# Optimization experiments

Hardware: AMD Instinct MI355X
Metric: run time of the kernel (lower is better)

The kernel has to match this reference:

```python
import jax, jax.numpy as jnp
import numpy as np
from jax import lax

BN_EPS = 1e-3  # Keras BatchNormalization default


def ste_sign(x):
    # larq ste_sign forward: +1 for x >= 0, -1 otherwise
    return jnp.where(x >= 0, 1.0, -1.0).astype(x.dtype)


def conv2d_valid(x, w):
    # x: NHWC, w: HWIO, stride 1, VALID padding
    return lax.conv_general_dilated(
        x, w, window_strides=(1, 1), padding='VALID',
        dimension_numbers=('NHWC', 'HWIO', 'NHWC'))


def maxpool2(x):
    return lax.reduce_window(x, -jnp.inf, lax.max,
                             (1, 2, 2, 1), (1, 2, 2, 1), 'VALID')


def bn_infer(x, mean, var, beta):
    # BatchNormalization(scale=False): center only
    return (x - mean) * lax.rsqrt(var + BN_EPS) + beta


def setup_inputs() -> dict:
    key = jax.random.key(0)
    ks = jax.random.split(key, 16)
    B, H, W, C = 256, 64, 64, 3
    inp = {
        'inputs': jax.random.normal(ks[0], (B, H, W, C), jnp.float32),
        'w1': jax.random.normal(ks[1], (3, 3, 3, 32), jnp.float32) * 0.1,
        'w2': jax.random.normal(ks[2], (3, 3, 32, 64), jnp.float32) * 0.1,
        'w3': jax.random.normal(ks[3], (3, 3, 64, 64), jnp.float32) * 0.1,
        'd1w': jax.random.normal(ks[4], (12 * 12 * 64, 64), jnp.float32) * 0.05,
        'd2w': jax.random.normal(ks[5], (64, 10), jnp.float32) * 0.1,
    }
    for i, (name, c) in enumerate([('bn1', 32), ('bn2', 64), ('bn3', 64), ('bn4', 64), ('bn5', 10)]):
        kk = jax.random.split(ks[6 + i], 3)
        inp[name + '_mean'] = jax.random.normal(kk[0], (c,), jnp.float32) * 0.1
        inp[name + '_var'] = jax.random.uniform(kk[1], (c,), jnp.float32, 0.5, 1.5)
        inp[name + '_beta'] = jax.random.normal(kk[2], (c,), jnp.float32) * 0.1
    return inp


def reference(inputs, w1, w2, w3, d1w, d2w,
              bn1_mean, bn1_var, bn1_beta,
              bn2_mean, bn2_var, bn2_beta,
              bn3_mean, bn3_var, bn3_beta,
              bn4_mean, bn4_var, bn4_beta,
              bn5_mean, bn5_var, bn5_beta):
    # conv1: kernel quantized only (no input quantizer)
    x = conv2d_valid(inputs, ste_sign(w1))           # [B,62,62,32]
    x = maxpool2(x)                                   # [B,31,31,32]
    x = bn_infer(x, bn1_mean, bn1_var, bn1_beta)
    # conv2: input + kernel quantized
    x = conv2d_valid(ste_sign(x), ste_sign(w2))       # [B,29,29,64]
    x = maxpool2(x)                                   # [B,14,14,64]
    x = bn_infer(x, bn2_mean, bn2_var, bn2_beta)
    x = conv2d_valid(ste_sign(x), ste_sign(w3))       # [B,12,12,64]
    x = bn_infer(x, bn3_mean, bn3_var, bn3_beta)
    x = x.reshape(x.shape[0], -1)                     # [B,9216]
    x = ste_sign(x) @ ste_sign(d1w)                   # [B,64]
    x = bn_infer(x, bn4_mean, bn4_var, bn4_beta)
    x = ste_sign(x) @ ste_sign(d2w)                   # [B,10]
    x = bn_infer(x, bn5_mean, bn5_var, bn5_beta)
    return jax.nn.softmax(x, axis=-1)
```

## Files before the change

kernel.cpp:

```cpp
#include <hip/hip_runtime.h>

typedef unsigned int u32;
typedef unsigned long long u64;

#define BN_EPS 1e-3f

static const size_t OFF_BITS1 = 0;
static const size_t OFF_BITS2 = 984064;
static const size_t OFF_W2B   = 1682432;
static const size_t OFF_W3B   = 1684736;
static const size_t OFF_D1WB  = 1689344;
static const size_t OFF_D2WB  = 1763072;
static const size_t OFF_T2    = 1763328;
static const size_t OFF_T3    = 1763584;
static const size_t OFF_T4    = 1763840;

__global__ __launch_bounds__(256) void k_head(
    const float* __restrict__ inp, const float* __restrict__ w1,
    const float* __restrict__ m1, const float* __restrict__ v1, const float* __restrict__ be1,
    const float* __restrict__ w2, const float* __restrict__ w3,
    const float* __restrict__ d1w, const float* __restrict__ d2w,
    const float* __restrict__ m2, const float* __restrict__ v2, const float* __restrict__ be2,
    const float* __restrict__ m3, const float* __restrict__ v3, const float* __restrict__ be3,
    const float* __restrict__ m4, const float* __restrict__ v4, const float* __restrict__ be4,
    u32* __restrict__ bits1,
    u32* __restrict__ w2b, u64* __restrict__ w3b, u64* __restrict__ d1wb,
    u64* __restrict__ d2wb, float* __restrict__ t2, float* __restrict__ t3,
    float* __restrict__ t4)
{
    int tid = threadIdx.x;

    if (blockIdx.x >= 961) {
        int pb = blockIdx.x - 961;
        if (pb < 36) {
            int idx = pb * 256 + tid;
            int wi = idx >> 6, oc = idx & 63;
            u64 bits = 0;
            for (int j = 0; j < 64; ++j)
                bits |= (u64)(d1w[(wi * 64 + j) * 64 + oc] >= 0.f) << j;
            d1wb[idx] = bits;
        } else if (pb < 39) {
            int idx = (pb - 36) * 256 + tid;
            if (idx < 576) {
                int tap = idx >> 6, oc = idx & 63;
                u32 bits = 0;
                for (int ic = 0; ic < 32; ++ic)
                    bits |= (u32)(w2[(tap * 32 + ic) * 64 + oc] >= 0.f) << ic;
                w2b[idx] = bits;
            }
        } else if (pb < 42) {
            int idx = (pb - 39) * 256 + tid;
            if (idx < 576) {
                int tap = idx >> 6, oc = idx & 63;
                u64 bits = 0;
                for (int ic = 0; ic < 64; ++ic)
                    bits |= (u64)(w3[(tap * 64 + ic) * 64 + oc] >= 0.f) << ic;
                w3b[idx] = bits;
            }
        } else {
            if (tid < 64)        t2[tid] = m2[tid] - be2[tid] * sqrtf(v2[tid] + BN_EPS);
            else if (tid < 128) { int c = tid - 64;  t3[c] = m3[c] - be3[c] * sqrtf(v3[c] + BN_EPS); }
            else if (tid < 192) { int c = tid - 128; t4[c] = m4[c] - be4[c] * sqrtf(v4[c] + BN_EPS); }
            else if (tid < 202) {
                int oc = tid - 192;
                u64 bits = 0;
                for (int j = 0; j < 64; ++j)
                    bits |= (u64)(d2w[j * 10 + oc] >= 0.f) << j;
                d2wb[oc] = bits;
            }
        }
        return;
    }

    __shared__ float wf[32 * 28];
    __shared__ float t1s[32];
    for (int i = tid; i < 864; i += 256) {
        int oc = i / 27, tap = i - oc * 27;
        wf[oc * 28 + tap] = (w1[tap * 32 + oc] >= 0.f) ? 1.f : -1.f;
    }
    if (tid < 32) t1s[tid] = m1[tid] - be1[tid] * sqrtf(v1[tid] + BN_EPS);
    __syncthreads();

    int gid = blockIdx.x * 256 + tid;
    int b = gid / 961;
    int p = gid - b * 961;
    int ph = p / 31, pw = p - ph * 31;

    float x[4][4][3];
    const float* base = inp + ((b * 64 + 2 * ph) * 64 + 2 * pw) * 3;
#pragma unroll
    for (int i = 0; i < 4; ++i)
#pragma unroll
        for (int j = 0; j < 4; ++j)
#pragma unroll
            for (int k = 0; k < 3; ++k)
                x[i][j][k] = base[(i * 64 + j) * 3 + k];

    u32 word = 0;
#pragma unroll 1
    for (int oc = 0; oc < 32; ++oc) {
        float wv[28];
        const float4* wq = reinterpret_cast<const float4*>(wf + oc * 28);
#pragma unroll
        for (int q = 0; q < 7; ++q) {
            float4 t = wq[q];
            wv[4 * q] = t.x; wv[4 * q + 1] = t.y; wv[4 * q + 2] = t.z; wv[4 * q + 3] = t.w;
        }
        float s00 = 0.f, s01 = 0.f, s10 = 0.f, s11 = 0.f;
#pragma unroll
        for (int ky = 0; ky < 3; ++ky)
#pragma unroll
            for (int kx = 0; kx < 3; ++kx)
#pragma unroll
                for (int ic = 0; ic < 3; ++ic) {
                    float w = wv[(ky * 3 + kx) * 3 + ic];
                    s00 = fmaf(w, x[ky][kx][ic], s00);
                    s01 = fmaf(w, x[ky][kx + 1][ic], s01);
                    s10 = fmaf(w, x[ky + 1][kx][ic], s10);
                    s11 = fmaf(w, x[ky + 1][kx + 1][ic], s11);
                }
        float m = fmaxf(fmaxf(s00, s01), fmaxf(s10, s11));
        if (m >= t1s[oc]) word |= (1u << oc);
    }
    bits1[gid] = word;
}

__global__ __launch_bounds__(256) void k_conv2(
    const u32* __restrict__ bits1, const u32* __restrict__ w2b,
    const float* __restrict__ t2, u64* __restrict__ bits2)
{
    int lane = threadIdx.x & 63;
    int wid = blockIdx.x * 4 + (threadIdx.x >> 6);
    int b = wid / 196;
    int p = wid - b * 196;
    int ph = p / 14, pw = p - ph * 14;

    const u32* xb = bits1 + b * 961 + (2 * ph) * 31 + 2 * pw;
    u32 xw[4][4];
#pragma unroll
    for (int i = 0; i < 4; ++i)
#pragma unroll
        for (int j = 0; j < 4; ++j)
            xw[i][j] = xb[i * 31 + j];

    u32 wv[9];
#pragma unroll
    for (int t = 0; t < 9; ++t) wv[t] = w2b[t * 64 + lane];

    int mn = 1 << 30;
#pragma unroll
    for (int dy = 0; dy < 2; ++dy)
#pragma unroll
        for (int dx = 0; dx < 2; ++dx) {
            int s = 0;
#pragma unroll
            for (int ky = 0; ky < 3; ++ky)
#pragma unroll
                for (int kx = 0; kx < 3; ++kx)
                    s += __popc(xw[dy + ky][dx + kx] ^ wv[ky * 3 + kx]);
            mn = min(mn, s);
        }
    float val = (float)(288 - 2 * mn);
    u64 word = __ballot(val >= t2[lane]);
    if (lane == 0) bits2[wid] = word;
}

__global__ __launch_bounds__(256) void k_tail(
    const u64* __restrict__ bits2, const u64* __restrict__ w3b,
    const float* __restrict__ t3, const u64* __restrict__ d1wb,
    const float* __restrict__ t4, const u64* __restrict__ d2wb,
    const float* __restrict__ m5, const float* __restrict__ v5,
    const float* __restrict__ be5, float* __restrict__ out)
{
    __shared__ u64 sb3[144];
    __shared__ int part[4][64];

    int tid  = threadIdx.x;
    int lane = tid & 63;
    int wv_  = tid >> 6;
    int b    = blockIdx.x;

    u64 wreg[9];
#pragma unroll
    for (int t = 0; t < 9; ++t) wreg[t] = w3b[t * 64 + lane];
    float t3v = t3[lane];

    const u64* ib = bits2 + b * 196;
#pragma unroll 2
    for (int i = 0; i < 36; ++i) {
        int pos = wv_ * 36 + i;
        int h = pos / 12, w = pos - h * 12;
        const u64* xb = ib + h * 14 + w;
        int s = 0;
#pragma unroll
        for (int ky = 0; ky < 3; ++ky)
#pragma unroll
            for (int kx = 0; kx < 3; ++kx)
                s += __popcll(xb[ky * 14 + kx] ^ wreg[ky * 3 + kx]);
        u64 word = __ballot((float)(576 - 2 * s) >= t3v);
        if (lane == 0) sb3[pos] = word;
    }
    __syncthreads();

    {
        int q = wv_, oc = lane;
        int s = 0;
#pragma unroll 6
        for (int i = 0; i < 36; ++i) {
            int w = q * 36 + i;
            s += __popcll(sb3[w] ^ d1wb[w * 64 + oc]);
        }
        part[q][oc] = s;
    }
    __syncthreads();

    if (tid < 64) {
        int s = part[0][tid] + part[1][tid] + part[2][tid] + part[3][tid];
        float val = (float)(9216 - 2 * s);
        u64 xv = __ballot(val >= t4[tid]);
        if (tid < 16) {
            int j = tid;
            bool ok = j < 10;
            float y = -1e30f;
            if (ok) {
                int v = 64 - 2 * (int)__popcll(xv ^ d2wb[j]);
                y = ((float)v - m5[j]) * rsqrtf(v5[j] + BN_EPS) + be5[j];
            }
            float mx = y;
#pragma unroll
            for (int off = 8; off >= 1; off >>= 1)
                mx = fmaxf(mx, __shfl_xor(mx, off, 16));
            float e = ok ? expf(y - mx) : 0.f;
            float sum = e;
#pragma unroll
            for (int off = 8; off >= 1; off >>= 1)
                sum += __shfl_xor(sum, off, 16);
            if (ok) out[b * 10 + j] = e / sum;
        }
    }
}

extern "C" void kernel_launch(void* const* d_in, const int* in_sizes, int n_in,
                              void* d_out, int out_size, void* d_ws, size_t ws_size,
                              hipStream_t stream)
{
    const float* inp = (const float*)d_in[0];
    const float* w1  = (const float*)d_in[1];
    const float* w2  = (const float*)d_in[2];
    const float* w3  = (const float*)d_in[3];
    const float* d1w = (const float*)d_in[4];
    const float* d2w = (const float*)d_in[5];
    const float* m1 = (const float*)d_in[6],  *v1 = (const float*)d_in[7],  *be1 = (const float*)d_in[8];
    const float* m2 = (const float*)d_in[9],  *v2 = (const float*)d_in[10], *be2 = (const float*)d_in[11];
    const float* m3 = (const float*)d_in[12], *v3 = (const float*)d_in[13], *be3 = (const float*)d_in[14];
    const float* m4 = (const float*)d_in[15], *v4 = (const float*)d_in[16], *be4 = (const float*)d_in[17];
    const float* m5 = (const float*)d_in[18], *v5 = (const float*)d_in[19], *be5 = (const float*)d_in[20];

    char* ws = (char*)d_ws;
    u32* bits1 = (u32*)(ws + OFF_BITS1);
    u64* bits2 = (u64*)(ws + OFF_BITS2);
    u32* w2b   = (u32*)(ws + OFF_W2B);
    u64* w3b   = (u64*)(ws + OFF_W3B);
    u64* d1wb  = (u64*)(ws + OFF_D1WB);
    u64* d2wb  = (u64*)(ws + OFF_D2WB);
    float* t2  = (float*)(ws + OFF_T2);
    float* t3  = (float*)(ws + OFF_T3);
    float* t4  = (float*)(ws + OFF_T4);

    k_head <<<1004,  256, 0, stream>>>(inp, w1, m1, v1, be1,
                                       w2, w3, d1w, d2w,
                                       m2, v2, be2, m3, v3, be3, m4, v4, be4,
                                       bits1, w2b, w3b, d1wb, d2wb, t2, t3, t4);
    k_conv2<<<12544, 256, 0, stream>>>(bits1, w2b, t2, bits2);
    k_tail <<<256,   256, 0, stream>>>(bits2, w3b, t3, d1wb, t4, d2wb,
                                       m5, v5, be5, (float*)d_out);
}
```

Measured before the change: 146.6 us.

## Fuse binary conv2 into tail kernel using shared-memory staging per image

Removes the separate conv2 kernel and computes the binarized conv2+maxpool inside the per-image tail block. Each block stages the image's bit-packed conv1 output in LDS, computes 196 pooled 64-bit words into shared memory, then proceeds with conv3 and the dense layers. This drops a kernel launch and the global round trip of the conv2 bitmap, at the cost of running conv2 on only 256 blocks (one per image), so there is less parallelism.

Result: no change. 147.4 us (+0.5%).

```diff
diff --git a/kernel.cpp b/kernel.cpp
--- a/kernel.cpp
+++ b/kernel.cpp
@@ -6,7 +6,6 @@
 #define BN_EPS 1e-3f
 
 static const size_t OFF_BITS1 = 0;
-static const size_t OFF_BITS2 = 984064;
 static const size_t OFF_W2B   = 1682432;
 static const size_t OFF_W3B   = 1684736;
 static const size_t OFF_D1WB  = 1689344;
@@ -125,53 +124,17 @@
     bits1[gid] = word;
 }
 
-__global__ __launch_bounds__(256) void k_conv2(
+__global__ __launch_bounds__(256) void k_tail(
     const u32* __restrict__ bits1, const u32* __restrict__ w2b,
-    const float* __restrict__ t2, u64* __restrict__ bits2)
-{
-    int lane = threadIdx.x & 63;
-    int wid = blockIdx.x * 4 + (threadIdx.x >> 6);
-    int b = wid / 196;
-    int p = wid - b * 196;
-    int ph = p / 14, pw = p - ph * 14;
-
-    const u32* xb = bits1 + b * 961 + (2 * ph) * 31 + 2 * pw;
-    u32 xw[4][4];
-#pragma unroll
-    for (int i = 0; i < 4; ++i)
-#pragma unroll
-        for (int j = 0; j < 4; ++j)
-            xw[i][j] = xb[i * 31 + j];
-
-    u32 wv[9];
-#pragma unroll
-    for (int t = 0; t < 9; ++t) wv[t] = w2b[t * 64 + lane];
-
-    int mn = 1 << 30;
-#pragma unroll
-    for (int dy = 0; dy < 2; ++dy)
-#pragma unroll
-        for (int dx = 0; dx < 2; ++dx) {
-            int s = 0;
-#pragma unroll
-            for (int ky = 0; ky < 3; ++ky)
-#pragma unroll
-                for (int kx = 0; kx < 3; ++kx)
-                    s += __popc(xw[dy + ky][dx + kx] ^ wv[ky * 3 + kx]);
-            mn = min(mn, s);
-        }
-    float val = (float)(288 - 2 * mn);
-    u64 word = __ballot(val >= t2[lane]);
-    if (lane == 0) bits2[wid] = word;
-}
-
-__global__ __launch_bounds__(256) void k_tail(
-    const u64* __restrict__ bits2, const u64* __restrict__ w3b,
-    const float* __restrict__ t3, const u64* __restrict__ d1wb,
-    const float* __restrict__ t4, const u64* __restrict__ d2wb,
+    const float* __restrict__ t2,
+    const u64* __restrict__ w3b, const float* __restrict__ t3,
+    const u64* __restrict__ d1wb, const float* __restrict__ t4,
+    const u64* __restrict__ d2wb,
     const float* __restrict__ m5, const float* __restrict__ v5,
     const float* __restrict__ be5, float* __restrict__ out)
 {
+    __shared__ u32 sb1[961];
+    __shared__ u64 sb2[196];
     __shared__ u64 sb3[144];
     __shared__ int part[4][64];
 
@@ -180,25 +143,60 @@
     int wv_  = tid >> 6;
     int b    = blockIdx.x;
 
-    u64 wreg[9];
-#pragma unroll
-    for (int t = 0; t < 9; ++t) wreg[t] = w3b[t * 64 + lane];
-    float t3v = t3[lane];
-
-    const u64* ib = bits2 + b * 196;
+    const u32* src = bits1 + b * 961;
+    for (int i = tid; i < 961; i += 256) sb1[i] = src[i];
+    __syncthreads();
+
+    {
+        u32 w2r[9];
+#pragma unroll
+        for (int t = 0; t < 9; ++t) w2r[t] = w2b[t * 64 + lane];
+        float t2v = t2[lane];
+
+#pragma unroll 1
+        for (int i = 0; i < 49; ++i) {
+            int p = wv_ * 49 + i;
+            int ph = p / 14, pw = p - ph * 14;
+            const u32* xb = &sb1[(2 * ph) * 31 + 2 * pw];
+            int mn = 1 << 30;
+#pragma unroll
+            for (int dy = 0; dy < 2; ++dy)
+#pragma unroll
+                for (int dx = 0; dx < 2; ++dx) {
+                    int s = 0;
+#pragma unroll
+                    for (int ky = 0; ky < 3; ++ky)
+#pragma unroll
+                        for (int kx = 0; kx < 3; ++kx)
+                            s += __popc(xb[(dy + ky) * 31 + dx + kx] ^ w2r[ky * 3 + kx]);
+                    mn = min(mn, s);
+                }
+            u64 word = __ballot((float)(288 - 2 * mn) >= t2v);
+            if (lane == 0) sb2[p] = word;
+        }
+    }
+    __syncthreads();
+
+    {
+        u64 wreg[9];
+#pragma unroll
+        for (int t = 0; t < 9; ++t) wreg[t] = w3b[t * 64 + lane];
+        float t3v = t3[lane];
+
 #pragma unroll 2
-    for (int i = 0; i < 36; ++i) {
-        int pos = wv_ * 36 + i;
-        int h = pos / 12, w = pos - h * 12;
-        const u64* xb = ib + h * 14 + w;
-        int s = 0;
-#pragma unroll
-        for (int ky = 0; ky < 3; ++ky)
-#pragma unroll
-            for (int kx = 0; kx < 3; ++kx)
-                s += __popcll(xb[ky * 14 + kx] ^ wreg[ky * 3 + kx]);
-        u64 word = __ballot((float)(576 - 2 * s) >= t3v);
-        if (lane == 0) sb3[pos] = word;
+        for (int i = 0; i < 36; ++i) {
+            int pos = wv_ * 36 + i;
+            int h = pos / 12, w = pos - h * 12;
+            const u64* xb = &sb2[h * 14 + w];
+            int s = 0;
+#pragma unroll
+            for (int ky = 0; ky < 3; ++ky)
+#pragma unroll
+                for (int kx = 0; kx < 3; ++kx)
+                    s += __popcll(xb[ky * 14 + kx] ^ wreg[ky * 3 + kx]);
+            u64 word = __ballot((float)(576 - 2 * s) >= t3v);
+            if (lane == 0) sb3[pos] = word;
+        }
     }
     __syncthreads();
 
@@ -258,7 +256,6 @@
 
     char* ws = (char*)d_ws;
     u32* bits1 = (u32*)(ws + OFF_BITS1);
-    u64* bits2 = (u64*)(ws + OFF_BITS2);
     u32* w2b   = (u32*)(ws + OFF_W2B);
     u64* w3b   = (u64*)(ws + OFF_W3B);
     u64* d1wb  = (u64*)(ws + OFF_D1WB);
@@ -267,11 +264,10 @@
     float* t3  = (float*)(ws + OFF_T3);
     float* t4  = (float*)(ws + OFF_T4);
 
-    k_head <<<1004,  256, 0, stream>>>(inp, w1, m1, v1, be1,
-                                       w2, w3, d1w, d2w,
-                                       m2, v2, be2, m3, v3, be3, m4, v4, be4,
-                                       bits1, w2b, w3b, d1wb, d2wb, t2, t3, t4);
-    k_conv2<<<12544, 256, 0, stream>>>(bits1, w2b, t2, bits2);
-    k_tail <<<256,   256, 0, stream>>>(bits2, w3b, t3, d1wb, t4, d2wb,
-                                       m5, v5, be5, (float*)d_out);
+    k_head <<<1004, 256, 0, stream>>>(inp, w1, m1, v1, be1,
+                                      w2, w3, d1w, d2w,
+                                      m2, v2, be2, m3, v3, be3, m4, v4, be4,
+                                      bits1, w2b, w3b, d1wb, d2wb, t2, t3, t4);
+    k_tail <<<256,  256, 0, stream>>>(bits1, w2b, t2, w3b, t3, d1wb, t4, d2wb,
+                                      m5, v5, be5, (float*)d_out);
 }
```
